# Kernel tuning notes

Measured on AMD Instinct MI355X. Metric: run time of the kernel, lower is better.

Reference implementation:

```python
import jax, jax.numpy as jnp
import numpy as np

B, T, D = 2, 4096, 512
H = 8
HD = D // H  # 64


def setup_inputs() -> dict:
    key = jax.random.key(0)
    k1, k2, k3 = jax.random.split(key, 3)
    x = jax.random.normal(k1, (B, T, D), dtype=jnp.float32)
    w_qkv = jax.random.normal(k2, (3 * D, D), dtype=jnp.float32) * (1.0 / np.sqrt(D))
    w_out = jax.random.normal(k3, (D, D), dtype=jnp.float32) * (1.0 / np.sqrt(D))
    return {"x": x, "w_qkv": w_qkv, "w_out": w_out}


def reference(x, w_qkv, w_out):
    b, t, d = x.shape
    qkv = x @ w_qkv.T                      # [B,T,3D]
    q, k, v = jnp.split(qkv, 3, axis=-1)
    # b t (h d) -> b h t d
    def split_heads(a):
        return a.reshape(b, t, H, HD).transpose(0, 2, 1, 3)
    q, k, v = split_heads(q), split_heads(k), split_heads(v)
    scale = 1.0 / np.sqrt(HD).astype(np.float32)
    scores = jnp.einsum('bhqd,bhkd->bhqk', q, k) * scale  # [B,H,T,T]
    causal = jnp.tril(jnp.ones((t, t), dtype=bool))        # keep lower triangle
    scores = jnp.where(causal[None, None], scores, -jnp.inf)
    attn = jax.nn.softmax(scores, axis=-1)
    out = jnp.einsum('bhqk,bhkd->bhqd', attn, v)           # [B,H,T,HD]
    out = out.transpose(0, 2, 1, 3).reshape(b, t, d)       # b h t d -> b t (h d)
    return out @ w_out.T
```

## Files before the change

kernel.cpp:

```cpp
#include <hip/hip_runtime.h>
#include <hip/hip_bf16.h>

#define BB 2
#define TT 4096
#define DD 512
#define HH 8
#define HD 64
#define M_TOT (BB*TT)
#define N_QKV (3*DD)

typedef __attribute__((ext_vector_type(8))) __bf16 bf16x8;
typedef __attribute__((ext_vector_type(4))) float f32x4;

#define MFMA32(a,b,c) __builtin_amdgcn_mfma_f32_16x16x32_bf16((a),(b),(c),0,0,0)

#define SCALE_L2E 0.18033688011112443f
#define SHIFT_L2E 11.541560327111707f

static __device__ __forceinline__ unsigned short f2bf(float f) {
    union { float f; unsigned u; } v; v.f = f;
    return (unsigned short)((v.u + 0x8000u) >> 16);
}
static __device__ __forceinline__ unsigned short f2bf_t(float f) {
    union { float f; unsigned u; } v; v.f = f;
    return (unsigned short)(v.u >> 16);
}

static __device__ __forceinline__ bf16x8 load8(const unsigned short* p) {
    bf16x8 v;
    __builtin_memcpy(&v, p, 16);
    return v;
}

static __device__ __forceinline__ bf16x8 ones_frag() {
    unsigned short u[8];
    #pragma unroll
    for (int i = 0; i < 8; i++) u[i] = 0x3F80;
    bf16x8 v; __builtin_memcpy(&v, u, 16);
    return v;
}

#define GLDS(gp, lp) __builtin_amdgcn_global_load_lds( \
    (const __attribute__((address_space(1))) unsigned int*)(gp), \
    (__attribute__((address_space(3))) unsigned int*)(lp), 16, 0, 0)

#define NX4 (M_TOT*DD/4)
#define NW4 (N_QKV*DD/4)
#define NO4 (DD*DD/4)
__global__ __launch_bounds__(256) void cast_all(
        const float* __restrict__ x, const float* __restrict__ wqkv,
        const float* __restrict__ wout,
        unsigned short* __restrict__ xb, unsigned short* __restrict__ wqkvb,
        unsigned short* __restrict__ woutb) {
    int i = blockIdx.x * 256 + threadIdx.x;
    const float* s; unsigned short* d; int j;
    if (i < NX4)            { s = x;    d = xb;    j = i; }
    else if (i < NX4 + NW4) { s = wqkv; d = wqkvb; j = i - NX4; }
    else                    { s = wout; d = woutb; j = i - NX4 - NW4; }
    float4 f = ((const float4*)s)[j];
    ushort4 o;
    o.x = f2bf(f.x); o.y = f2bf(f.y); o.z = f2bf(f.z); o.w = f2bf(f.w);
    ((ushort4*)d)[j] = o;
}

__global__ __launch_bounds__(256) void qkv_gemm(
        const unsigned short* __restrict__ xb,
        const unsigned short* __restrict__ wb,
        unsigned short* __restrict__ qb,
        unsigned short* __restrict__ kb,
        unsigned short* __restrict__ vtb) {
    __shared__ union {
        struct { unsigned short As[2][128 * 32]; unsigned short Bs[2][128 * 32]; } g;
        unsigned short vt[4][64][72];
    } sm;
    int tid = threadIdx.x;
    int w = tid >> 6, lane = tid & 63;
    int lrow = lane & 15, quad = lane >> 4;
    int wg = (blockIdx.x & 7) * 96 + (blockIdx.x >> 3);
    int bn = wg % (N_QKV / 128);
    int bm = wg / (N_QKV / 128);
    int m0 = bm * 128, n0 = bn * 128;
    int wm = w >> 1, wn = w & 1;

    f32x4 c[4][4];
    #pragma unroll
    for (int i = 0; i < 4; i++)
        #pragma unroll
        for (int j = 0; j < 4; j++) c[i][j] = (f32x4){0.f, 0.f, 0.f, 0.f};

#define QSTAGE(buf, k0s) {                                                    \
    _Pragma("unroll")                                                         \
    for (int j = 0; j < 2; j++) {                                             \
        int ch = j * 256 + tid;                                               \
        int row = ch >> 2, kc = ch & 3;                                       \
        GLDS(xb + (size_t)(m0 + row) * DD + (k0s) + kc * 8,                   \
             (char*)sm.g.As[buf] + (size_t)(j * 256 + w * 64) * 16);          \
    }                                                                         \
    _Pragma("unroll")                                                         \
    for (int j = 0; j < 2; j++) {                                             \
        int ch = j * 256 + tid;                                               \
        int row = ch >> 2, kc = ch & 3;                                       \
        GLDS(wb + (size_t)(n0 + row) * DD + (k0s) + kc * 8,                   \
             (char*)sm.g.Bs[buf] + (size_t)(j * 256 + w * 64) * 16);          \
    } }

    QSTAGE(0, 0);
    __syncthreads();
    #pragma unroll 2
    for (int t = 0; t < 16; t++) {
        int cur = t & 1;
        if (t < 15) QSTAGE(cur ^ 1, (t + 1) * 32);
        bf16x8 a[4], b[4];
        #pragma unroll
        for (int mf = 0; mf < 4; mf++) a[mf] = load8(&sm.g.As[cur][(wm * 64 + mf * 16 + lrow) * 32 + quad * 8]);
        #pragma unroll
        for (int nf = 0; nf < 4; nf++) b[nf] = load8(&sm.g.Bs[cur][(wn * 64 + nf * 16 + lrow) * 32 + quad * 8]);
        #pragma unroll
        for (int mf = 0; mf < 4; mf++)
            #pragma unroll
            for (int nf = 0; nf < 4; nf++)
                c[mf][nf] = MFMA32(a[mf], b[nf], c[mf][nf]);
        __syncthreads();
    }
#undef QSTAGE

    int m0w = m0 + wm * 64, n0w = n0 + wn * 64;
    int which = n0w >> 9;
    int h = (n0w & 511) >> 6;
    if (which < 2) {
        unsigned short* dst = (which == 0) ? qb : kb;
        #pragma unroll
        for (int mf = 0; mf < 4; mf++) {
            #pragma unroll
            for (int r = 0; r < 4; r++) {
                int m = m0w + mf * 16 + quad * 4 + r;
                int t = m & (TT - 1), bi = m >> 12;
                size_t hb = (size_t)(bi * HH + h) * TT + t;
                #pragma unroll
                for (int nf = 0; nf < 4; nf++)
                    dst[hb * HD + nf * 16 + lrow] = f2bf(c[mf][nf][r]);
            }
        }
    } else {
        #pragma unroll
        for (int mf = 0; mf < 4; mf++)
            #pragma unroll
            for (int r = 0; r < 4; r++)
                #pragma unroll
                for (int nf = 0; nf < 4; nf++)
                    sm.vt[w][nf * 16 + lrow][mf * 16 + quad * 4 + r] = f2bf(c[mf][nf][r]);
        int bi = m0w >> 12, t0 = m0w & (TT - 1);
        size_t hb = (size_t)(bi * HH + h) * HD;
        #pragma unroll
        for (int i = 0; i < 8; i++) {
            int d = i * 8 + (lane >> 3);
            int tc = (lane & 7) * 8;
            bf16x8 v;
            __builtin_memcpy(&v, &sm.vt[w][d][tc], 16);
            __builtin_memcpy(vtb + (hb + d) * TT + t0 + tc, &v, 16);
        }
    }
}

__global__ __launch_bounds__(256) void attn_kernel(
        const unsigned short* __restrict__ qb,
        const unsigned short* __restrict__ kb,
        const unsigned short* __restrict__ vtb,
        unsigned short* __restrict__ attnb) {
    __shared__ union {
        unsigned short p[4][64][68];
        float c[2][64][66];
    } sm;

    const f32x4 ZERO4 = {0.f, 0.f, 0.f, 0.f};
    int w = threadIdx.x >> 6;
    int lane = threadIdx.x & 63;
    int lrow = lane & 15, quad = lane >> 4;
    int bh = blockIdx.x & 15;
    int qt = 63 - (blockIdx.x >> 4);
    int bi = bh >> 3, h = bh & 7;
    int q0 = qt * 64;

    const unsigned short* qh = qb + (size_t)bh * TT * HD;
    const unsigned short* kh = kb + (size_t)bh * TT * HD;
    const unsigned short* vth = vtb + (size_t)bh * HD * TT;
    bf16x8 ones = ones_frag();

    bf16x8 qf[4][2];
    #pragma unroll
    for (int mf = 0; mf < 4; mf++) {
        const unsigned short* qp = qh + (q0 + mf * 16 + lrow) * HD + quad * 8;
        qf[mf][0] = load8(qp);
        qf[mf][1] = load8(qp + 32);
    }

    f32x4 o[4][4];
    f32x4 l[4];
    #pragma unroll
    for (int i = 0; i < 4; i++) {
        l[i] = ZERO4;
        #pragma unroll
        for (int j = 0; j < 4; j++) o[i][j] = ZERO4;
    }

    for (int kt = w; kt <= qt; kt += 4) {
        int kbase = kt * 64;
        bool diag = (kt == qt);
        bf16x8 kf[4][2], vf[4][2];
        #pragma unroll
        for (int nf = 0; nf < 4; nf++) {
            const unsigned short* kp = kh + (kbase + nf * 16 + lrow) * HD + quad * 8;
            kf[nf][0] = load8(kp);
            kf[nf][1] = load8(kp + 32);
            const unsigned short* vp = vth + (nf * 16 + lrow) * TT + kbase + quad * 8;
            vf[nf][0] = load8(vp);
            vf[nf][1] = load8(vp + 32);
        }
        #pragma unroll
        for (int mf = 0; mf < 4; mf++) {
            #pragma unroll
            for (int nf = 0; nf < 4; nf++) {
                if (diag && nf > mf) {
                    #pragma unroll
                    for (int r = 0; r < 4; r++)
                        sm.p[w][mf * 16 + quad * 4 + r][nf * 16 + lrow] = 0;
                } else {
                    f32x4 s = MFMA32(qf[mf][0], kf[nf][0], ZERO4);
                    s = MFMA32(qf[mf][1], kf[nf][1], s);
                    #pragma unroll
                    for (int r = 0; r < 4; r++) {
                        float p = __builtin_amdgcn_exp2f(s[r] * SCALE_L2E - SHIFT_L2E);
                        if (diag && nf == mf && lrow > quad * 4 + r) p = 0.f;
                        sm.p[w][mf * 16 + quad * 4 + r][nf * 16 + lrow] = f2bf_t(p);
                    }
                }
            }
            bf16x8 pa0, pa1;
            __builtin_memcpy(&pa0, &sm.p[w][mf * 16 + lrow][quad * 8], 16);
            __builtin_memcpy(&pa1, &sm.p[w][mf * 16 + lrow][32 + quad * 8], 16);
            l[mf] = MFMA32(pa0, ones, l[mf]);
            l[mf] = MFMA32(pa1, ones, l[mf]);
            #pragma unroll
            for (int nfd = 0; nfd < 4; nfd++) {
                o[mf][nfd] = MFMA32(pa0, vf[nfd][0], o[mf][nfd]);
                o[mf][nfd] = MFMA32(pa1, vf[nfd][1], o[mf][nfd]);
            }
        }
    }

    __syncthreads();
    if (w >= 2) {
        int cb = w - 2;
        #pragma unroll
        for (int mf = 0; mf < 4; mf++)
            #pragma unroll
            for (int r = 0; r < 4; r++) {
                int row = mf * 16 + quad * 4 + r;
                #pragma unroll
                for (int nfd = 0; nfd < 4; nfd++)
                    sm.c[cb][row][nfd * 16 + lrow] = o[mf][nfd][r];
                if (lrow == 0) sm.c[cb][row][64] = l[mf][r];
            }
    }
    __syncthreads();
    if (w < 2) {
        #pragma unroll
        for (int mf = 0; mf < 4; mf++)
            #pragma unroll
            for (int r = 0; r < 4; r++) {
                int row = mf * 16 + quad * 4 + r;
                #pragma unroll
                for (int nfd = 0; nfd < 4; nfd++)
                    sm.c[w][row][nfd * 16 + lrow] += o[mf][nfd][r];
                if (lrow == 0) sm.c[w][row][64] += l[mf][r];
            }
    }
    __syncthreads();
    {
        int q = threadIdx.x >> 2, dseg = (threadIdx.x & 3) * 16;
        const float* r0 = &sm.c[0][q][0];
        const float* r1 = &sm.c[1][q][0];
        float inv = 1.0f / (r0[64] + r1[64]);
        unsigned outp[8];
        #pragma unroll
        for (int i = 0; i < 8; i++) {
            float a0 = (r0[dseg + 2 * i] + r1[dseg + 2 * i]) * inv;
            float a1 = (r0[dseg + 2 * i + 1] + r1[dseg + 2 * i + 1]) * inv;
            outp[i] = (unsigned)f2bf_t(a0) | ((unsigned)f2bf_t(a1) << 16);
        }
        unsigned short* dst = attnb + ((size_t)(bi * TT + q0 + q)) * DD + h * HD + dseg;
        __builtin_memcpy(dst, outp, 16);
        __builtin_memcpy(dst + 8, outp + 4, 16);
    }
}

__global__ __launch_bounds__(256) void proj_gemm(
        const unsigned short* __restrict__ ab,
        const unsigned short* __restrict__ wb,
        float* __restrict__ out) {
    __shared__ unsigned short As[2][64 * 32];
    __shared__ unsigned short Bs[2][128 * 32];
    int tid = threadIdx.x;
    int w = tid >> 6, lane = tid & 63;
    int lrow = lane & 15, quad = lane >> 4;
    int bn = blockIdx.x % (DD / 128);
    int bm = blockIdx.x / (DD / 128);
    int m0 = bm * 64, n0 = bn * 128;

    f32x4 c[4][2];
    #pragma unroll
    for (int i = 0; i < 4; i++)
        #pragma unroll
        for (int j = 0; j < 2; j++) c[i][j] = (f32x4){0.f, 0.f, 0.f, 0.f};

#define PSTAGE(buf, k0s) {                                                    \
    {                                                                         \
        int ch = tid;                                                         \
        int row = ch >> 2, kc = ch & 3;                                       \
        GLDS(ab + (size_t)(m0 + row) * DD + (k0s) + kc * 8,                   \
             (char*)As[buf] + (size_t)(w * 64) * 16);                         \
    }                                                                         \
    _Pragma("unroll")                                                         \
    for (int j = 0; j < 2; j++) {                                             \
        int ch = j * 256 + tid;                                               \
        int row = ch >> 2, kc = ch & 3;                                       \
        GLDS(wb + (size_t)(n0 + row) * DD + (k0s) + kc * 8,                   \
             (char*)Bs[buf] + (size_t)(j * 256 + w * 64) * 16);               \
    } }

    PSTAGE(0, 0);
    __syncthreads();
    #pragma unroll 2
    for (int t = 0; t < 16; t++) {
        int cur = t & 1;
        if (t < 15) PSTAGE(cur ^ 1, (t + 1) * 32);
        bf16x8 a[4], b[2];
        #pragma unroll
        for (int mf = 0; mf < 4; mf++) a[mf] = load8(&As[cur][(mf * 16 + lrow) * 32 + quad * 8]);
        #pragma unroll
        for (int nf = 0; nf < 2; nf++) b[nf] = load8(&Bs[cur][(w * 32 + nf * 16 + lrow) * 32 + quad * 8]);
        #pragma unroll
        for (int mf = 0; mf < 4; mf++)
            #pragma unroll
            for (int nf = 0; nf < 2; nf++)
                c[mf][nf] = MFMA32(a[mf], b[nf], c[mf][nf]);
        __syncthreads();
    }
#undef PSTAGE

    #pragma unroll
    for (int mf = 0; mf < 4; mf++) {
        #pragma unroll
        for (int r = 0; r < 4; r++) {
            int m = m0 + mf * 16 + quad * 4 + r;
            #pragma unroll
            for (int nf = 0; nf < 2; nf++) {
                int n = n0 + w * 32 + nf * 16 + lrow;
                out[(size_t)m * DD + n] = c[mf][nf][r];
            }
        }
    }
}

extern "C" void kernel_launch(void* const* d_in, const int* in_sizes, int n_in,
                              void* d_out, int out_size, void* d_ws, size_t ws_size,
                              hipStream_t stream) {
    const float* x    = (const float*)d_in[0];
    const float* wqkv = (const float*)d_in[1];
    const float* wout = (const float*)d_in[2];
    float* out = (float*)d_out;

    char* ws = (char*)d_ws;
    unsigned short* xb    = (unsigned short*)ws; ws += (size_t)M_TOT * DD * 2;
    unsigned short* wqkvb = (unsigned short*)ws; ws += (size_t)N_QKV * DD * 2;
    unsigned short* woutb = (unsigned short*)ws; ws += (size_t)DD * DD * 2;
    unsigned short* qb    = (unsigned short*)ws; ws += (size_t)BB * HH * TT * HD * 2;
    unsigned short* kb    = (unsigned short*)ws; ws += (size_t)BB * HH * TT * HD * 2;
    unsigned short* vtb   = (unsigned short*)ws; ws += (size_t)BB * HH * HD * TT * 2;
    unsigned short* attnb = (unsigned short*)ws; ws += (size_t)M_TOT * DD * 2;

    cast_all<<<(NX4 + NW4 + NO4) / 256, 256, 0, stream>>>(x, wqkv, wout, xb, wqkvb, woutb);

    qkv_gemm<<<(M_TOT / 128) * (N_QKV / 128), 256, 0, stream>>>(xb, wqkvb, qb, kb, vtb);

    attn_kernel<<<1024, 256, 0, stream>>>(qb, kb, vtb, attnb);

    proj_gemm<<<(M_TOT / 64) * (DD / 128), 256, 0, stream>>>(attnb, woutb, out);
}
```

Measured before the change: 182.2 us.

## Restructure attention to row-split warps with double-buffered LDS K/V staging

The attention kernel changes its work split. Each warp now owns 16 query rows and walks every key tile, instead of each warp owning a strided subset of key tiles across all 64 rows and then reducing partial sums through shared memory. K and V tiles are staged into XOR-swizzled, double-buffered shared memory using a direct global-to-LDS copy, prefetching the next tile while the current one is computed. This removes the cross-warp reduction and the redundant per-warp K/V global loads, at the cost of a block barrier every key tile and scattered 2-byte output stores.

Result: no change. 180.8 us (-0.8%).

```diff
diff --git a/kernel.cpp b/kernel.cpp
--- a/kernel.cpp
+++ b/kernel.cpp
@@ -167,14 +167,13 @@
         const unsigned short* __restrict__ kb,
         const unsigned short* __restrict__ vtb,
         unsigned short* __restrict__ attnb) {
-    __shared__ union {
-        unsigned short p[4][64][68];
-        float c[2][64][66];
-    } sm;
+    __shared__ unsigned short Ks[2][64 * 64];
+    __shared__ unsigned short Vs[2][64 * 64];
+    __shared__ unsigned short Ps[4][16 * 64];
 
     const f32x4 ZERO4 = {0.f, 0.f, 0.f, 0.f};
-    int w = threadIdx.x >> 6;
-    int lane = threadIdx.x & 63;
+    int tid = threadIdx.x;
+    int w = tid >> 6, lane = tid & 63;
     int lrow = lane & 15, quad = lane >> 4;
     int bh = blockIdx.x & 15;
     int qt = 63 - (blockIdx.x >> 4);
@@ -186,111 +185,96 @@
     const unsigned short* vth = vtb + (size_t)bh * HD * TT;
     bf16x8 ones = ones_frag();
 
-    bf16x8 qf[4][2];
-    #pragma unroll
-    for (int mf = 0; mf < 4; mf++) {
-        const unsigned short* qp = qh + (q0 + mf * 16 + lrow) * HD + quad * 8;
-        qf[mf][0] = load8(qp);
-        qf[mf][1] = load8(qp + 32);
-    }
-
-    f32x4 o[4][4];
-    f32x4 l[4];
-    #pragma unroll
-    for (int i = 0; i < 4; i++) {
-        l[i] = ZERO4;
-        #pragma unroll
-        for (int j = 0; j < 4; j++) o[i][j] = ZERO4;
-    }
-
-    for (int kt = w; kt <= qt; kt += 4) {
-        int kbase = kt * 64;
+    bf16x8 qf0, qf1;
+    {
+        const unsigned short* qp = qh + (size_t)(q0 + w * 16 + lrow) * HD + quad * 8;
+        qf0 = load8(qp);
+        qf1 = load8(qp + 32);
+    }
+
+    int s0 = tid, s1 = 256 + tid;
+    int r0 = s0 >> 3, c0 = ((s0 & 7) ^ (r0 & 7)) * 8;
+    int r1 = s1 >> 3, c1 = ((s1 & 7) ^ (r1 & 7)) * 8;
+
+#define STAGE(buf, kt_) {                                                     \
+    int kb_ = (kt_) * 64;                                                     \
+    GLDS(kh + (size_t)(kb_ + r0) * HD + c0, (char*)Ks[buf] + w * 1024);       \
+    GLDS(kh + (size_t)(kb_ + r1) * HD + c1, (char*)Ks[buf] + 4096 + w * 1024);\
+    GLDS(vth + (size_t)r0 * TT + kb_ + c0,  (char*)Vs[buf] + w * 1024);       \
+    GLDS(vth + (size_t)r1 * TT + kb_ + c1,  (char*)Vs[buf] + 4096 + w * 1024);\
+    }
+
+    f32x4 o[4];
+    f32x4 l = ZERO4;
+    #pragma unroll
+    for (int i = 0; i < 4; i++) o[i] = ZERO4;
+
+    int sw = lrow & 7;
+    int blo = (quad ^ sw) * 8;
+    int bhi = ((quad + 4) ^ sw) * 8;
+
+    STAGE(0, 0);
+    __syncthreads();
+    int buf = 0;
+    for (int kt = 0; kt <= qt; kt++) {
+        if (kt < qt) STAGE(buf ^ 1, kt + 1);
         bool diag = (kt == qt);
-        bf16x8 kf[4][2], vf[4][2];
+
         #pragma unroll
         for (int nf = 0; nf < 4; nf++) {
-            const unsigned short* kp = kh + (kbase + nf * 16 + lrow) * HD + quad * 8;
-            kf[nf][0] = load8(kp);
-            kf[nf][1] = load8(kp + 32);
-            const unsigned short* vp = vth + (nf * 16 + lrow) * TT + kbase + quad * 8;
-            vf[nf][0] = load8(vp);
-            vf[nf][1] = load8(vp + 32);
-        }
-        #pragma unroll
-        for (int mf = 0; mf < 4; mf++) {
-            #pragma unroll
-            for (int nf = 0; nf < 4; nf++) {
-                if (diag && nf > mf) {
-                    #pragma unroll
-                    for (int r = 0; r < 4; r++)
-                        sm.p[w][mf * 16 + quad * 4 + r][nf * 16 + lrow] = 0;
-                } else {
-                    f32x4 s = MFMA32(qf[mf][0], kf[nf][0], ZERO4);
-                    s = MFMA32(qf[mf][1], kf[nf][1], s);
-                    #pragma unroll
-                    for (int r = 0; r < 4; r++) {
-                        float p = __builtin_amdgcn_exp2f(s[r] * SCALE_L2E - SHIFT_L2E);
-                        if (diag && nf == mf && lrow > quad * 4 + r) p = 0.f;
-                        sm.p[w][mf * 16 + quad * 4 + r][nf * 16 + lrow] = f2bf_t(p);
-                    }
+            if (diag && nf > w) {
+                #pragma unroll
+                for (int r = 0; r < 4; r++) {
+                    int row = quad * 4 + r, col = nf * 16 + lrow;
+                    Ps[w][row * 64 + ((((col >> 3) ^ (row & 7)) << 3) | (col & 7))] = 0;
+                }
+            } else {
+                int krow = nf * 16 + lrow;
+                bf16x8 k0, k1;
+                __builtin_memcpy(&k0, &Ks[buf][krow * 64 + blo], 16);
+                __builtin_memcpy(&k1, &Ks[buf][krow * 64 + bhi], 16);
+                f32x4 s = MFMA32(qf0, k0, ZERO4);
+                s = MFMA32(qf1, k1, s);
+                #pragma unroll
+                for (int r = 0; r < 4; r++) {
+                    float p = __builtin_amdgcn_exp2f(s[r] * SCALE_L2E - SHIFT_L2E);
+                    if (diag && nf == w && lrow > quad * 4 + r) p = 0.f;
+                    int row = quad * 4 + r, col = nf * 16 + lrow;
+                    Ps[w][row * 64 + ((((col >> 3) ^ (row & 7)) << 3) | (col & 7))] = f2bf_t(p);
                 }
             }
-            bf16x8 pa0, pa1;
-            __builtin_memcpy(&pa0, &sm.p[w][mf * 16 + lrow][quad * 8], 16);
-            __builtin_memcpy(&pa1, &sm.p[w][mf * 16 + lrow][32 + quad * 8], 16);
-            l[mf] = MFMA32(pa0, ones, l[mf]);
-            l[mf] = MFMA32(pa1, ones, l[mf]);
-            #pragma unroll
-            for (int nfd = 0; nfd < 4; nfd++) {
-                o[mf][nfd] = MFMA32(pa0, vf[nfd][0], o[mf][nfd]);
-                o[mf][nfd] = MFMA32(pa1, vf[nfd][1], o[mf][nfd]);
-            }
-        }
-    }
-
-    __syncthreads();
-    if (w >= 2) {
-        int cb = w - 2;
-        #pragma unroll
-        for (int mf = 0; mf < 4; mf++)
-            #pragma unroll
-            for (int r = 0; r < 4; r++) {
-                int row = mf * 16 + quad * 4 + r;
-                #pragma unroll
-                for (int nfd = 0; nfd < 4; nfd++)
-                    sm.c[cb][row][nfd * 16 + lrow] = o[mf][nfd][r];
-                if (lrow == 0) sm.c[cb][row][64] = l[mf][r];
-            }
-    }
-    __syncthreads();
-    if (w < 2) {
-        #pragma unroll
-        for (int mf = 0; mf < 4; mf++)
-            #pragma unroll
-            for (int r = 0; r < 4; r++) {
-                int row = mf * 16 + quad * 4 + r;
-                #pragma unroll
-                for (int nfd = 0; nfd < 4; nfd++)
-                    sm.c[w][row][nfd * 16 + lrow] += o[mf][nfd][r];
-                if (lrow == 0) sm.c[w][row][64] += l[mf][r];
-            }
-    }
-    __syncthreads();
-    {
-        int q = threadIdx.x >> 2, dseg = (threadIdx.x & 3) * 16;
-        const float* r0 = &sm.c[0][q][0];
-        const float* r1 = &sm.c[1][q][0];
-        float inv = 1.0f / (r0[64] + r1[64]);
-        unsigned outp[8];
-        #pragma unroll
-        for (int i = 0; i < 8; i++) {
-            float a0 = (r0[dseg + 2 * i] + r1[dseg + 2 * i]) * inv;
-            float a1 = (r0[dseg + 2 * i + 1] + r1[dseg + 2 * i + 1]) * inv;
-            outp[i] = (unsigned)f2bf_t(a0) | ((unsigned)f2bf_t(a1) << 16);
-        }
-        unsigned short* dst = attnb + ((size_t)(bi * TT + q0 + q)) * DD + h * HD + dseg;
-        __builtin_memcpy(dst, outp, 16);
-        __builtin_memcpy(dst + 8, outp + 4, 16);
+        }
+
+        bf16x8 pa0, pa1;
+        __builtin_memcpy(&pa0, &Ps[w][lrow * 64 + blo], 16);
+        __builtin_memcpy(&pa1, &Ps[w][lrow * 64 + bhi], 16);
+        __builtin_amdgcn_s_setprio(1);
+        l = MFMA32(pa0, ones, l);
+        l = MFMA32(pa1, ones, l);
+        #pragma unroll
+        for (int nfd = 0; nfd < 4; nfd++) {
+            int vrow = nfd * 16 + lrow;
+            bf16x8 v0, v1;
+            __builtin_memcpy(&v0, &Vs[buf][vrow * 64 + blo], 16);
+            __builtin_memcpy(&v1, &Vs[buf][vrow * 64 + bhi], 16);
+            o[nfd] = MFMA32(pa0, v0, o[nfd]);
+            o[nfd] = MFMA32(pa1, v1, o[nfd]);
+        }
+        __builtin_amdgcn_s_setprio(0);
+
+        __syncthreads();
+        buf ^= 1;
+    }
+#undef STAGE
+
+    #pragma unroll
+    for (int r = 0; r < 4; r++) {
+        float inv = 1.0f / l[r];
+        int m = bi * TT + q0 + w * 16 + quad * 4 + r;
+        unsigned short* dst = attnb + (size_t)m * DD + h * HD + lrow;
+        #pragma unroll
+        for (int nfd = 0; nfd < 4; nfd++)
+            dst[nfd * 16] = f2bf_t(o[nfd][r] * inv);
     }
 }
 
```
